# Kernel optimization log

Measured on AMD Instinct MI355X. Metric: run time of the kernel, lower is better.

Reference implementation:

```python
import jax, jax.numpy as jnp
import numpy as np

B, S, D_MODEL = 2, 2048, 2048
N_HEADS, N_KV_HEADS, HEAD_DIM = 32, 8, 64
N_GROUPS = N_HEADS // N_KV_HEADS


def setup_inputs() -> dict:
    key = jax.random.key(0)
    ks = jax.random.split(key, 5)
    x = jax.random.normal(ks[0], (B, S, D_MODEL), dtype=jnp.float32)
    wq = jax.random.normal(ks[1], (N_HEADS * HEAD_DIM, D_MODEL), dtype=jnp.float32) * 0.02
    wk = jax.random.normal(ks[2], (N_KV_HEADS * HEAD_DIM, D_MODEL), dtype=jnp.float32) * 0.02
    wv = jax.random.normal(ks[3], (N_KV_HEADS * HEAD_DIM, D_MODEL), dtype=jnp.float32) * 0.02
    wo = jax.random.normal(ks[4], (D_MODEL, N_HEADS * HEAD_DIM), dtype=jnp.float32) * 0.02
    # Rotary tables: module's apply_rope expects cos/sin of shape [S, head_dim//2]
    half = HEAD_DIM // 2
    inv_freq = 1.0 / (10000.0 ** (jnp.arange(0, half, dtype=jnp.float32) / half))
    angles = jnp.arange(S, dtype=jnp.float32)[:, None] * inv_freq[None, :]  # [S, half]
    cos = jnp.cos(angles)
    sin = jnp.sin(angles)
    return {"x": x, "wq": wq, "wk": wk, "wv": wv, "wo": wo, "cos": cos, "sin": sin}


def _rotate_half(t):
    half = t.shape[-1] // 2
    return jnp.concatenate((-t[..., half:], t[..., :half]), axis=-1)


def _apply_rope(q, k, cos, sin):
    # cos/sin: [S, head_dim//2] -> repeat_interleave(2) -> [S, head_dim]
    cos2 = jnp.repeat(cos, 2, axis=-1)[None, :, None, :]  # [1,S,1,D]
    sin2 = jnp.repeat(sin, 2, axis=-1)[None, :, None, :]
    q_rot = q * cos2 + _rotate_half(q) * sin2
    k_rot = k * cos2 + _rotate_half(k) * sin2
    return q_rot, k_rot


def reference(x, wq, wk, wv, wo, cos, sin):
    b, s, _ = x.shape
    q = (x @ wq.T).reshape(b, s, N_HEADS, HEAD_DIM)
    k = (x @ wk.T).reshape(b, s, N_KV_HEADS, HEAD_DIM)
    v = (x @ wv.T).reshape(b, s, N_KV_HEADS, HEAD_DIM)
    q, k = _apply_rope(q, k, cos, sin)
    # GQA expansion: repeat_interleave along head dim
    k = jnp.repeat(k, N_GROUPS, axis=2)  # [b,s,H,D]
    v = jnp.repeat(v, N_GROUPS, axis=2)
    q = q.transpose(0, 2, 1, 3)  # [b,H,s,D]
    k = k.transpose(0, 2, 1, 3)
    v = v.transpose(0, 2, 1, 3)
    scale = HEAD_DIM ** -0.5
    scores = jnp.einsum("bhqd,bhkd->bhqk", q, k) * scale
    causal = jnp.tril(jnp.ones((s, s), dtype=bool))
    scores = jnp.where(causal[None, None], scores, jnp.finfo(scores.dtype).min)
    attn = jax.nn.softmax(scores, axis=-1)
    out = jnp.einsum("bhqk,bhkd->bhqd", attn, v)
    out = out.transpose(0, 2, 1, 3).reshape(b, s, N_HEADS * HEAD_DIM)
    return out @ wo.T
```

## Files before the change

### kernel.cpp

```cpp
#include <hip/hip_runtime.h>
#include <hip/hip_bf16.h>

#define B_   2
#define S_   2048
#define DM   2048
#define NH   32
#define NKV  8
#define HD   64
#define MROWS 4096
#define NQKV  3072

typedef __attribute__((ext_vector_type(8))) short bf16x8;
typedef __attribute__((ext_vector_type(4))) float f32x4;
typedef __attribute__((ext_vector_type(16))) float f32x16;

__device__ __forceinline__ unsigned short f2b(float f) {
  __hip_bfloat16 h = __float2bfloat16(f);
  return *reinterpret_cast<unsigned short*>(&h);
}

__device__ __forceinline__ void gload16(const void* g, void* l) {
  __builtin_amdgcn_global_load_lds((__attribute__((address_space(1))) void*)g,
                                   (__attribute__((address_space(3))) void*)l,
                                   16, 0, 0);
}

__device__ __forceinline__ unsigned cvtpk(float lo, float hi) {
  unsigned r;
  asm("v_cvt_pk_bf16_f32 %0, %1, %2" : "=v"(r) : "v"(lo), "v"(hi));
  return r;
}

__device__ __forceinline__ void pl32swap(unsigned& a, unsigned& b) {
  asm volatile("v_permlane32_swap_b32 %0, %1" : "+v"(a), "+v"(b));
}

__device__ __forceinline__ float exp2hw(float x) {
  float r;
  asm("v_exp_f32 %0, %1" : "=v"(r) : "v"(x));
  return r;
}

__device__ __forceinline__ bf16x8 mk8(unsigned w0, unsigned w1, unsigned w2, unsigned w3) {
  union { unsigned u[4]; bf16x8 v; } uu;
  uu.u[0] = w0; uu.u[1] = w1; uu.u[2] = w2; uu.u[3] = w3;
  return uu.v;
}

__global__ __launch_bounds__(256) void f2bf_kernel(const float* __restrict__ in,
                                                   unsigned short* __restrict__ out, int n4) {
  int i = blockIdx.x * 256 + threadIdx.x;
  if (i < n4) {
    float4 v = reinterpret_cast<const float4*>(in)[i];
    ushort4 o;
    o.x = f2b(v.x); o.y = f2b(v.y); o.z = f2b(v.z); o.w = f2b(v.w);
    reinterpret_cast<ushort4*>(out)[i] = o;
  }
}

__global__ __launch_bounds__(256) void wcat_kernel(const float* __restrict__ wq,
                                                   const float* __restrict__ wk,
                                                   const float* __restrict__ wv,
                                                   unsigned short* __restrict__ out) {
  int i = blockIdx.x * 256 + threadIdx.x;
  int e = i * 4;
  int row = e >> 11;
  int col = e & 2047;
  const float* src;
  if (row < 2048)      src = wq + (size_t)row * 2048 + col;
  else if (row < 2560) src = wk + (size_t)(row - 2048) * 2048 + col;
  else                 src = wv + (size_t)(row - 2560) * 2048 + col;
  float4 v = *reinterpret_cast<const float4*>(src);
  ushort4 o;
  o.x = f2b(v.x); o.y = f2b(v.y); o.z = f2b(v.z); o.w = f2b(v.w);
  reinterpret_cast<ushort4*>(out)[i] = o;
}

#define BMg 256
#define BNg 128
#define BKg 64
#define QSCALE 0.18033688011112042f

__global__ __launch_bounds__(512, 2) void gemm_qkv(const unsigned short* __restrict__ A,
                                                   const unsigned short* __restrict__ Bm,
                                                   unsigned short* __restrict__ Qb,
                                                   unsigned short* __restrict__ Kb2,
                                                   unsigned short* __restrict__ Vtb,
                                                   const float* __restrict__ cosg,
                                                   const float* __restrict__ sing) {
  const int K = DM;
  __shared__ unsigned short Abuf[3][BMg * BKg];
  __shared__ unsigned short Bbuf[3][BNg * BKg];
  const int tid = threadIdx.x;
  const int wave = tid >> 6, lane = tid & 63;
  const int wr = wave >> 1, wc = wave & 1;
  const int rowbase = blockIdx.y * BMg;
  const int colbase = blockIdx.x * BNg;
  const unsigned short* Ag = A + (size_t)rowbase * K;
  const unsigned short* Bg = Bm + (size_t)colbase * K;
  const int NT = K / BKg;

  auto stage_half = [&](int buf, int k0, int half) {
#pragma unroll
    for (int i = 0; i < 2; ++i) {
      int c = wave * 256 + (half * 2 + i) * 64 + lane;
      int r = c >> 3, p = c & 7;
      gload16(Ag + (size_t)r * K + k0 + ((p ^ (r & 7)) << 3),
              &Abuf[buf][(wave * 256 + (half * 2 + i) * 64) * 8]);
    }
    int c = wave * 128 + half * 64 + lane;
    int r = c >> 3, p = c & 7;
    gload16(Bg + (size_t)r * K + k0 + ((p ^ (r & 7)) << 3),
            &Bbuf[buf][(wave * 128 + half * 64) * 8]);
  };
  auto ldA = [&](int buf, int row, int c16) -> bf16x8 {
    return *(const bf16x8*)((const char*)&Abuf[buf][0] + row * 128 + ((c16 ^ (row & 7)) << 4));
  };
  auto ldB = [&](int buf, int row, int c16) -> bf16x8 {
    return *(const bf16x8*)((const char*)&Bbuf[buf][0] + row * 128 + ((c16 ^ (row & 7)) << 4));
  };

  f32x4 acc[4][4];
#pragma unroll
  for (int a = 0; a < 4; a++)
#pragma unroll
    for (int b2 = 0; b2 < 4; b2++) acc[a][b2] = (f32x4){0.f, 0.f, 0.f, 0.f};

  const int l15 = lane & 15, l4 = lane >> 4;

  stage_half(0, 0, 0); stage_half(0, 0, 1);
  stage_half(1, BKg, 0); stage_half(1, BKg, 1);
  asm volatile("s_waitcnt vmcnt(6)" ::: "memory");
  __builtin_amdgcn_s_barrier();

  int cur = 0;
  for (int t = 0; t < NT; ++t) {
    const int nxt2 = (cur >= 1) ? cur - 1 : cur + 2;
    {
      bf16x8 af[4], bfv[4];
#pragma unroll
      for (int mt = 0; mt < 4; ++mt) af[mt] = ldA(cur, wr * 64 + mt * 16 + l15, l4);
#pragma unroll
      for (int nt = 0; nt < 4; ++nt) bfv[nt] = ldB(cur, wc * 64 + nt * 16 + l15, l4);
      if (t + 2 < NT) stage_half(nxt2, (t + 2) * BKg, 0);
      __builtin_amdgcn_s_barrier();
      __builtin_amdgcn_s_setprio(1);
#pragma unroll
      for (int mt = 0; mt < 4; ++mt)
#pragma unroll
        for (int nt = 0; nt < 4; ++nt)
          acc[mt][nt] = __builtin_amdgcn_mfma_f32_16x16x32_bf16(af[mt], bfv[nt], acc[mt][nt], 0, 0, 0);
      __builtin_amdgcn_s_setprio(0);
      __builtin_amdgcn_s_barrier();
    }
    {
      bf16x8 af[4], bfv[4];
#pragma unroll
      for (int mt = 0; mt < 4; ++mt) af[mt] = ldA(cur, wr * 64 + mt * 16 + l15, 4 + l4);
#pragma unroll
      for (int nt = 0; nt < 4; ++nt) bfv[nt] = ldB(cur, wc * 64 + nt * 16 + l15, 4 + l4);
      if (t + 2 < NT) stage_half(nxt2, (t + 2) * BKg, 1);
      __builtin_amdgcn_s_barrier();
      __builtin_amdgcn_s_setprio(1);
#pragma unroll
      for (int mt = 0; mt < 4; ++mt)
#pragma unroll
        for (int nt = 0; nt < 4; ++nt)
          acc[mt][nt] = __builtin_amdgcn_mfma_f32_16x16x32_bf16(af[mt], bfv[nt], acc[mt][nt], 0, 0, 0);
      __builtin_amdgcn_s_setprio(0);
      if (t < NT - 1) {
        if (t + 2 < NT) asm volatile("s_waitcnt vmcnt(6)" ::: "memory");
        else            asm volatile("s_waitcnt vmcnt(0)" ::: "memory");
        __builtin_amdgcn_s_barrier();
      }
    }
    cur = (cur < 2) ? cur + 1 : 0;
  }

  const int orow = rowbase + wr * 64, ocol = colbase + wc * 64;
  if (colbase < 2048) {
#pragma unroll
    for (int mt = 0; mt < 4; ++mt)
#pragma unroll
      for (int r = 0; r < 4; ++r) {
        const int row = orow + mt * 16 + l4 * 4 + r;
        const int s = row & 2047;
        const float* cR = cosg + s * 32;
        const float* sR = sing + s * 32;
#pragma unroll
        for (int nt = 0; nt < 2; ++nt) {
          const int i2 = nt * 8 + (l15 >> 1);
          float c0 = cR[i2], sv0 = sR[i2], c1 = cR[16 + i2], sv1 = sR[16 + i2];
          float alo = acc[mt][nt][r], ahi = acc[mt][nt + 2][r];
          size_t base = (size_t)row * 2048 + ocol + nt * 16 + l15;
          Qb[base]      = f2b((alo * c0 - ahi * sv0) * QSCALE);
          Qb[base + 32] = f2b((ahi * c1 + alo * sv1) * QSCALE);
        }
      }
  } else if (colbase < 2560) {
    const int kcol = ocol - 2048;
#pragma unroll
    for (int mt = 0; mt < 4; ++mt)
#pragma unroll
      for (int r = 0; r < 4; ++r) {
        const int row = orow + mt * 16 + l4 * 4 + r;
        const int s = row & 2047;
        const float* cR = cosg + s * 32;
        const float* sR = sing + s * 32;
#pragma unroll
        for (int nt = 0; nt < 2; ++nt) {
          const int i2 = nt * 8 + (l15 >> 1);
          float c0 = cR[i2], sv0 = sR[i2], c1 = cR[16 + i2], sv1 = sR[16 + i2];
          float alo = acc[mt][nt][r], ahi = acc[mt][nt + 2][r];
          size_t base = (size_t)row * 512 + kcol + nt * 16 + l15;
          Kb2[base]      = f2b(alo * c0 - ahi * sv0);
          Kb2[base + 32] = f2b(ahi * c1 + alo * sv1);
        }
      }
  } else {
    const int hkv = (ocol - 2560) >> 6;
#pragma unroll
    for (int mt = 0; mt < 4; ++mt)
#pragma unroll
      for (int nt = 0; nt < 4; ++nt) {
        const int d = nt * 16 + l15;
        const int row0 = orow + mt * 16 + l4 * 4;
        const int b = row0 >> 11, s0i = row0 & 2047;
        ushort4 u;
        u.x = f2b(acc[mt][nt][0]); u.y = f2b(acc[mt][nt][1]);
        u.z = f2b(acc[mt][nt][2]); u.w = f2b(acc[mt][nt][3]);
        *(ushort4*)(Vtb + ((size_t)(b * NKV + hkv) * HD + d) * S_ + s0i) = u;
      }
  }
}

__global__ __launch_bounds__(512, 2) void gemm_bt(const unsigned short* __restrict__ A,
                                                  const unsigned short* __restrict__ Bm,
                                                  float* __restrict__ C,
                                                  int M, int N, int K) {
  __shared__ unsigned short Abuf[3][BMg * BKg];
  __shared__ unsigned short Bbuf[3][BNg * BKg];
  const int tid = threadIdx.x;
  const int wave = tid >> 6, lane = tid & 63;
  const int wr = wave >> 1, wc = wave & 1;
  const int rowbase = blockIdx.y * BMg;
  const int colbase = blockIdx.x * BNg;
  const unsigned short* Ag = A + (size_t)rowbase * K;
  const unsigned short* Bg = Bm + (size_t)colbase * K;
  const int NT = K / BKg;

  auto stage_half = [&](int buf, int k0, int half) {
#pragma unroll
    for (int i = 0; i < 2; ++i) {
      int c = wave * 256 + (half * 2 + i) * 64 + lane;
      int r = c >> 3, p = c & 7;
      gload16(Ag + (size_t)r * K + k0 + ((p ^ (r & 7)) << 3),
              &Abuf[buf][(wave * 256 + (half * 2 + i) * 64) * 8]);
    }
    int c = wave * 128 + half * 64 + lane;
    int r = c >> 3, p = c & 7;
    gload16(Bg + (size_t)r * K + k0 + ((p ^ (r & 7)) << 3),
            &Bbuf[buf][(wave * 128 + half * 64) * 8]);
  };
  auto ldA = [&](int buf, int row, int c16) -> bf16x8 {
    return *(const bf16x8*)((const char*)&Abuf[buf][0] + row * 128 + ((c16 ^ (row & 7)) << 4));
  };
  auto ldB = [&](int buf, int row, int c16) -> bf16x8 {
    return *(const bf16x8*)((const char*)&Bbuf[buf][0] + row * 128 + ((c16 ^ (row & 7)) << 4));
  };

  f32x4 acc[4][4];
#pragma unroll
  for (int a = 0; a < 4; a++)
#pragma unroll
    for (int b2 = 0; b2 < 4; b2++) acc[a][b2] = (f32x4){0.f, 0.f, 0.f, 0.f};

  const int l15 = lane & 15, l4 = lane >> 4;

  stage_half(0, 0, 0); stage_half(0, 0, 1);
  stage_half(1, BKg, 0); stage_half(1, BKg, 1);
  asm volatile("s_waitcnt vmcnt(6)" ::: "memory");
  __builtin_amdgcn_s_barrier();

  int cur = 0;
  for (int t = 0; t < NT; ++t) {
    const int nxt2 = (cur >= 1) ? cur - 1 : cur + 2;
    {
      bf16x8 af[4], bfv[4];
#pragma unroll
      for (int mt = 0; mt < 4; ++mt) af[mt] = ldA(cur, wr * 64 + mt * 16 + l15, l4);
#pragma unroll
      for (int nt = 0; nt < 4; ++nt) bfv[nt] = ldB(cur, wc * 64 + nt * 16 + l15, l4);
      if (t + 2 < NT) stage_half(nxt2, (t + 2) * BKg, 0);
      __builtin_amdgcn_s_barrier();
      __builtin_amdgcn_s_setprio(1);
#pragma unroll
      for (int mt = 0; mt < 4; ++mt)
#pragma unroll
        for (int nt = 0; nt < 4; ++nt)
          acc[mt][nt] = __builtin_amdgcn_mfma_f32_16x16x32_bf16(af[mt], bfv[nt], acc[mt][nt], 0, 0, 0);
      __builtin_amdgcn_s_setprio(0);
      __builtin_amdgcn_s_barrier();
    }
    {
      bf16x8 af[4], bfv[4];
#pragma unroll
      for (int mt = 0; mt < 4; ++mt) af[mt] = ldA(cur, wr * 64 + mt * 16 + l15, 4 + l4);
#pragma unroll
      for (int nt = 0; nt < 4; ++nt) bfv[nt] = ldB(cur, wc * 64 + nt * 16 + l15, 4 + l4);
      if (t + 2 < NT) stage_half(nxt2, (t + 2) * BKg, 1);
      __builtin_amdgcn_s_barrier();
      __builtin_amdgcn_s_setprio(1);
#pragma unroll
      for (int mt = 0; mt < 4; ++mt)
#pragma unroll
        for (int nt = 0; nt < 4; ++nt)
          acc[mt][nt] = __builtin_amdgcn_mfma_f32_16x16x32_bf16(af[mt], bfv[nt], acc[mt][nt], 0, 0, 0);
      __builtin_amdgcn_s_setprio(0);
      if (t < NT - 1) {
        if (t + 2 < NT) asm volatile("s_waitcnt vmcnt(6)" ::: "memory");
        else            asm volatile("s_waitcnt vmcnt(0)" ::: "memory");
        __builtin_amdgcn_s_barrier();
      }
    }
    cur = (cur < 2) ? cur + 1 : 0;
  }

  const int orow = rowbase + wr * 64, ocol = colbase + wc * 64;
#pragma unroll
  for (int mt = 0; mt < 4; mt++)
#pragma unroll
    for (int nt = 0; nt < 4; nt++)
#pragma unroll
      for (int r = 0; r < 4; r++)
        C[(size_t)(orow + mt * 16 + l4 * 4 + r) * N + ocol + nt * 16 + l15] = acc[mt][nt][r];
}

__global__ __launch_bounds__(256) void attn_kernel(const unsigned short* __restrict__ Qb,
                                                   const unsigned short* __restrict__ Kb2,
                                                   const unsigned short* __restrict__ Vt,
                                                   unsigned short* __restrict__ AO) {
  const int pr = blockIdx.x, h = blockIdx.y, b = blockIdx.z;
  const int hk = h >> 2;
  __shared__ unsigned short Kbuf[3][4096];
  __shared__ unsigned short Vbuf[3][4096];
  const int tid = threadIdx.x, wave = tid >> 6, lane = tid & 63;
  const int l31 = lane & 31, hi = lane >> 5;

  const unsigned short* Qrow = Qb + (size_t)b * S_ * 2048 + h * 64;
  const unsigned short* Krow = Kb2 + (size_t)b * S_ * 512 + hk * 64;
  const unsigned short* Vbase = Vt + (size_t)(b * NKV + hk) * HD * S_;

  const int NT_B = 2 * (16 - pr);
  const int NTtot = 34;

  auto j0_of = [&](int tl) { return (tl < NT_B ? tl : tl - NT_B) * 64; };
  auto stage = [&](int j0, int bufi) {
#pragma unroll
    for (int tt = 0; tt < 2; ++tt) {
      int slot = (wave * 2 + tt) * 64 + lane;
      int row = slot >> 3, blk = slot & 7;
      int sb = ((blk ^ (row & 7)) << 3);
      gload16(Krow + (size_t)(j0 + row) * 512 + sb, &Kbuf[bufi][(wave * 2 + tt) * 512]);
      gload16(Vbase + (size_t)row * S_ + j0 + sb, &Vbuf[bufi][(wave * 2 + tt) * 512]);
    }
  };

  stage(0, 0);
  stage(j0_of(1), 1);
  asm volatile("s_waitcnt vmcnt(4)" ::: "memory");
  __builtin_amdgcn_s_barrier();

  int cur = 0, tlin = 0;

  for (int rg = 0; rg < 2; ++rg) {
    const int qbi = rg == 0 ? (15 - pr) : pr;
    const int qb = qbi * 128;
    const int NT = 2 * (qbi + 1);
    const int q0w = qb + wave * 32;
    const int qg = q0w + l31;

    bf16x8 qf[4];
#pragma unroll
    for (int c = 0; c < 4; ++c)
      qf[c] = *reinterpret_cast<const bf16x8*>(Qrow + (size_t)qg * 2048 + c * 16 + hi * 8);

    f32x16 Oa0 = {}, Oa1 = {};
    float m_old = -INFINITY, lsum = 0.f;

    for (int t = 0; t < NT; ++t, ++tlin) {
      const int j0 = t * 64;
      if (tlin + 2 < NTtot) stage(j0_of(tlin + 2), cur >= 1 ? cur - 1 : cur + 2);

      if (j0 < q0w + 32) {
        const char* Klc = (const char*)&Kbuf[cur][0];
        const char* Vlc = (const char*)&Vbuf[cur][0];

        f32x16 s0 = {}, s1 = {};
        __builtin_amdgcn_s_setprio(1);
#pragma unroll
        for (int c = 0; c < 4; ++c) {
          const int r0 = l31;
          bf16x8 kf = *(const bf16x8*)(Klc + r0 * 128 + ((((c << 1) + hi) ^ (r0 & 7)) << 4));
          s0 = __builtin_amdgcn_mfma_f32_32x32x16_bf16(kf, qf[c], s0, 0, 0, 0);
        }
#pragma unroll
        for (int c = 0; c < 4; ++c) {
          const int r1 = 32 + l31;
          bf16x8 kf = *(const bf16x8*)(Klc + r1 * 128 + ((((c << 1) + hi) ^ (r1 & 7)) << 4));
          s1 = __builtin_amdgcn_mfma_f32_32x32x16_bf16(kf, qf[c], s1, 0, 0, 0);
        }
        __builtin_amdgcn_s_setprio(0);

        const bool need_mask = (j0 + 63 > q0w);
        const int kb0 = j0 + 4 * hi, kb1 = j0 + 32 + 4 * hi;
        if (need_mask) {
#pragma unroll
          for (int r = 0; r < 16; ++r) {
            const int ko = (r & 3) + 8 * (r >> 2);
            if (kb0 + ko > qg) s0[r] = -INFINITY;
            if (kb1 + ko > qg) s1[r] = -INFINITY;
          }
        }

        float a0 = fmaxf(s0[0], s1[0]), a1 = fmaxf(s0[1], s1[1]);
        float a2 = fmaxf(s0[2], s1[2]), a3 = fmaxf(s0[3], s1[3]);
#pragma unroll
        for (int r = 4; r < 16; r += 4) {
          a0 = fmaxf(a0, fmaxf(s0[r], s1[r]));
          a1 = fmaxf(a1, fmaxf(s0[r + 1], s1[r + 1]));
          a2 = fmaxf(a2, fmaxf(s0[r + 2], s1[r + 2]));
          a3 = fmaxf(a3, fmaxf(s0[r + 3], s1[r + 3]));
        }
        float mxt = fmaxf(fmaxf(a0, a1), fmaxf(a2, a3));
        mxt = fmaxf(mxt, __shfl_xor(mxt, 32, 64));

        if (!__all(mxt - m_old <= 8.f)) {
          float mnew = fmaxf(m_old, mxt);
          float corr = exp2hw(m_old - mnew);
          m_old = mnew;
          lsum *= corr;
#pragma unroll
          for (int r = 0; r < 16; ++r) { Oa0[r] *= corr; Oa1[r] *= corr; }
        }

        float t0 = 0.f, t1 = 0.f, t2 = 0.f, t3 = 0.f;
#pragma unroll
        for (int r = 0; r < 16; r += 4) {
          s0[r]     = exp2hw(s0[r] - m_old);     t0 += s0[r];
          s0[r + 1] = exp2hw(s0[r + 1] - m_old); t1 += s0[r + 1];
          s0[r + 2] = exp2hw(s0[r + 2] - m_old); t2 += s0[r + 2];
          s0[r + 3] = exp2hw(s0[r + 3] - m_old); t3 += s0[r + 3];
        }
#pragma unroll
        for (int r = 0; r < 16; r += 4) {
          s1[r]     = exp2hw(s1[r] - m_old);     t0 += s1[r];
          s1[r + 1] = exp2hw(s1[r + 1] - m_old); t1 += s1[r + 1];
          s1[r + 2] = exp2hw(s1[r + 2] - m_old); t2 += s1[r + 2];
          s1[r + 3] = exp2hw(s1[r + 3] - m_old); t3 += s1[r + 3];
        }
        float rs = (t0 + t1) + (t2 + t3);
        rs += __shfl_xor(rs, 32, 64);
        lsum += rs;

        unsigned a0u = cvtpk(s0[0], s0[1]),  b0u = cvtpk(s0[4], s0[5]);  pl32swap(a0u, b0u);
        unsigned a1u = cvtpk(s0[2], s0[3]),  b1u = cvtpk(s0[6], s0[7]);  pl32swap(a1u, b1u);
        bf16x8 pf00 = mk8(a0u, a1u, b0u, b1u);
        unsigned a2u = cvtpk(s0[8], s0[9]),  b2u = cvtpk(s0[12], s0[13]); pl32swap(a2u, b2u);
        unsigned a3u = cvtpk(s0[10], s0[11]), b3u = cvtpk(s0[14], s0[15]); pl32swap(a3u, b3u);
        bf16x8 pf01 = mk8(a2u, a3u, b2u, b3u);
        unsigned a4u = cvtpk(s1[0], s1[1]),  b4u = cvtpk(s1[4], s1[5]);  pl32swap(a4u, b4u);
        unsigned a5u = cvtpk(s1[2], s1[3]),  b5u = cvtpk(s1[6], s1[7]);  pl32swap(a5u, b5u);
        bf16x8 pf10 = mk8(a4u, a5u, b4u, b5u);
        unsigned a6u = cvtpk(s1[8], s1[9]),  b6u = cvtpk(s1[12], s1[13]); pl32swap(a6u, b6u);
        unsigned a7u = cvtpk(s1[10], s1[11]), b7u = cvtpk(s1[14], s1[15]); pl32swap(a7u, b7u);
        bf16x8 pf11 = mk8(a6u, a7u, b6u, b7u);

        __builtin_amdgcn_s_setprio(1);
#pragma unroll
        for (int sk = 0; sk < 4; ++sk) {
          const int s = sk >> 1, kc = sk & 1;
          const bf16x8 pf = (sk == 0) ? pf00 : (sk == 1) ? pf01 : (sk == 2) ? pf10 : pf11;
          {
            const int row = l31;
            bf16x8 vf = *(const bf16x8*)(Vlc + row * 128 +
                          ((((s << 2) + (kc << 1) + hi) ^ (row & 7)) << 4));
            Oa0 = __builtin_amdgcn_mfma_f32_32x32x16_bf16(vf, pf, Oa0, 0, 0, 0);
          }
          {
            const int row = 32 + l31;
            bf16x8 vf = *(const bf16x8*)(Vlc + row * 128 +
                          ((((s << 2) + (kc << 1) + hi) ^ (row & 7)) << 4));
            Oa1 = __builtin_amdgcn_mfma_f32_32x32x16_bf16(vf, pf, Oa1, 0, 0, 0);
          }
        }
        __builtin_amdgcn_s_setprio(0);
      }

      if (tlin + 1 < NTtot) {
        if (tlin + 2 < NTtot) asm volatile("s_waitcnt vmcnt(4)" ::: "memory");
        else                  asm volatile("s_waitcnt vmcnt(0)" ::: "memory");
        __builtin_amdgcn_s_barrier();
      }
      cur = (cur < 2) ? cur + 1 : 0;
    }

    const float inv = 1.0f / lsum;
    unsigned short* ob = AO + (size_t)(b * S_ + qg) * 2048 + h * 64;
#pragma unroll
    for (int c = 0; c < 4; ++c) {
      ushort4 u0, u1;
      u0.x = f2b(Oa0[4 * c] * inv);     u0.y = f2b(Oa0[4 * c + 1] * inv);
      u0.z = f2b(Oa0[4 * c + 2] * inv); u0.w = f2b(Oa0[4 * c + 3] * inv);
      u1.x = f2b(Oa1[4 * c] * inv);     u1.y = f2b(Oa1[4 * c + 1] * inv);
      u1.z = f2b(Oa1[4 * c + 2] * inv); u1.w = f2b(Oa1[4 * c + 3] * inv);
      *(ushort4*)(ob + 8 * c + 4 * hi)      = u0;
      *(ushort4*)(ob + 32 + 8 * c + 4 * hi) = u1;
    }
  }
}

extern "C" void kernel_launch(void* const* d_in, const int* in_sizes, int n_in,
                              void* d_out, int out_size, void* d_ws, size_t ws_size,
                              hipStream_t stream) {
  (void)in_sizes; (void)n_in; (void)out_size; (void)ws_size;
  const float* x    = (const float*)d_in[0];
  const float* wq   = (const float*)d_in[1];
  const float* wk   = (const float*)d_in[2];
  const float* wv   = (const float*)d_in[3];
  const float* wo   = (const float*)d_in[4];
  const float* wo_  = wo;
  const float* cosg = (const float*)d_in[5];
  const float* sing = (const float*)d_in[6];
  (void)wo_;

  char* ws = (char*)d_ws;
  unsigned short* xb   = (unsigned short*)(ws);
  unsigned short* wcat = (unsigned short*)(ws + 16777216);
  unsigned short* wob  = (unsigned short*)(ws + 29360128);
  unsigned short* Qb   = (unsigned short*)(ws + 37748736);
  unsigned short* Kb2  = (unsigned short*)(ws + 54525952);
  unsigned short* Vtb  = (unsigned short*)(ws + 58720256);
  unsigned short* AO   = xb;

  f2bf_kernel<<<8192, 256, 0, stream>>>(x, xb, 2097152);
  wcat_kernel<<<6144, 256, 0, stream>>>(wq, wk, wv, wcat);
  f2bf_kernel<<<4096, 256, 0, stream>>>(wo, wob, 1048576);

  gemm_qkv<<<dim3(NQKV / BNg, MROWS / BMg), 512, 0, stream>>>(xb, wcat, Qb, Kb2, Vtb, cosg, sing);

  attn_kernel<<<dim3(8, NH, B_), 256, 0, stream>>>(Qb, Kb2, Vtb, AO);

  gemm_bt<<<dim3(DM / BNg, MROWS / BMg), 512, 0, stream>>>(AO, wob, (float*)d_out, MROWS, DM, DM);
}
```

Before: 203.6 us.

## Retile QKV GEMM to 128x128x32 and widen attention KV tiles to 128

The QKV projection GEMM moves from 256x128x64 tiles with 512 threads to 128x128x32 tiles with 256 threads. This gives more blocks (768 instead of 192) and targets higher occupancy, at the cost of more barriers per unit of K. Separately, the attention kernel now processes 128-key tiles with double buffering instead of 64-key tiles with triple buffering. That halves the number of loop iterations and barriers, but raises register pressure from four score accumulators and doubles the shared memory per stage. The prefetch is now issued after a barrier at the end of each iteration, rather than at the start.

New measurement: 184.3 us. 1.1x faster.

```diff
diff --git a/kernel.cpp b/kernel.cpp
--- a/kernel.cpp
+++ b/kernel.cpp
@@ -76,12 +76,9 @@
   reinterpret_cast<ushort4*>(out)[i] = o;
 }
 
-#define BMg 256
-#define BNg 128
-#define BKg 64
 #define QSCALE 0.18033688011112042f
 
-__global__ __launch_bounds__(512, 2) void gemm_qkv(const unsigned short* __restrict__ A,
+__global__ __launch_bounds__(256, 3) void gemm_qkv(const unsigned short* __restrict__ A,
                                                    const unsigned short* __restrict__ Bm,
                                                    unsigned short* __restrict__ Qb,
                                                    unsigned short* __restrict__ Kb2,
@@ -89,35 +86,38 @@
                                                    const float* __restrict__ cosg,
                                                    const float* __restrict__ sing) {
   const int K = DM;
-  __shared__ unsigned short Abuf[3][BMg * BKg];
-  __shared__ unsigned short Bbuf[3][BNg * BKg];
+  __shared__ unsigned short Abuf[3][128 * 32];
+  __shared__ unsigned short Bbuf[3][128 * 32];
   const int tid = threadIdx.x;
   const int wave = tid >> 6, lane = tid & 63;
   const int wr = wave >> 1, wc = wave & 1;
-  const int rowbase = blockIdx.y * BMg;
-  const int colbase = blockIdx.x * BNg;
+  const int rowbase = blockIdx.y * 128;
+  const int colbase = blockIdx.x * 128;
   const unsigned short* Ag = A + (size_t)rowbase * K;
   const unsigned short* Bg = Bm + (size_t)colbase * K;
-  const int NT = K / BKg;
-
-  auto stage_half = [&](int buf, int k0, int half) {
-#pragma unroll
-    for (int i = 0; i < 2; ++i) {
-      int c = wave * 256 + (half * 2 + i) * 64 + lane;
-      int r = c >> 3, p = c & 7;
-      gload16(Ag + (size_t)r * K + k0 + ((p ^ (r & 7)) << 3),
-              &Abuf[buf][(wave * 256 + (half * 2 + i) * 64) * 8]);
-    }
-    int c = wave * 128 + half * 64 + lane;
-    int r = c >> 3, p = c & 7;
-    gload16(Bg + (size_t)r * K + k0 + ((p ^ (r & 7)) << 3),
-            &Bbuf[buf][(wave * 128 + half * 64) * 8]);
-  };
-  auto ldA = [&](int buf, int row, int c16) -> bf16x8 {
-    return *(const bf16x8*)((const char*)&Abuf[buf][0] + row * 128 + ((c16 ^ (row & 7)) << 4));
-  };
-  auto ldB = [&](int buf, int row, int c16) -> bf16x8 {
-    return *(const bf16x8*)((const char*)&Bbuf[buf][0] + row * 128 + ((c16 ^ (row & 7)) << 4));
+  const int NT = K / 32;
+
+  auto stage = [&](int buf, int k0) {
+#pragma unroll
+    for (int it = 0; it < 2; ++it) {
+      int slot = wave * 128 + it * 64 + lane;
+      int r = slot >> 2, p = slot & 3;
+      gload16(Ag + (size_t)r * K + k0 + ((p ^ ((r >> 1) & 3)) << 3),
+              &Abuf[buf][(wave * 128 + it * 64) * 8]);
+    }
+#pragma unroll
+    for (int it = 0; it < 2; ++it) {
+      int slot = wave * 128 + it * 64 + lane;
+      int r = slot >> 2, p = slot & 3;
+      gload16(Bg + (size_t)r * K + k0 + ((p ^ ((r >> 1) & 3)) << 3),
+              &Bbuf[buf][(wave * 128 + it * 64) * 8]);
+    }
+  };
+  auto ldA = [&](int buf, int row, int c) -> bf16x8 {
+    return *(const bf16x8*)((const char*)&Abuf[buf][0] + row * 64 + ((c ^ ((row >> 1) & 3)) << 4));
+  };
+  auto ldB = [&](int buf, int row, int c) -> bf16x8 {
+    return *(const bf16x8*)((const char*)&Bbuf[buf][0] + row * 64 + ((c ^ ((row >> 1) & 3)) << 4));
   };
 
   f32x4 acc[4][4];
@@ -128,51 +128,32 @@
 
   const int l15 = lane & 15, l4 = lane >> 4;
 
-  stage_half(0, 0, 0); stage_half(0, 0, 1);
-  stage_half(1, BKg, 0); stage_half(1, BKg, 1);
-  asm volatile("s_waitcnt vmcnt(6)" ::: "memory");
+  stage(0, 0);
+  stage(1, 32);
+  asm volatile("s_waitcnt vmcnt(4)" ::: "memory");
   __builtin_amdgcn_s_barrier();
 
   int cur = 0;
   for (int t = 0; t < NT; ++t) {
     const int nxt2 = (cur >= 1) ? cur - 1 : cur + 2;
-    {
-      bf16x8 af[4], bfv[4];
-#pragma unroll
-      for (int mt = 0; mt < 4; ++mt) af[mt] = ldA(cur, wr * 64 + mt * 16 + l15, l4);
-#pragma unroll
-      for (int nt = 0; nt < 4; ++nt) bfv[nt] = ldB(cur, wc * 64 + nt * 16 + l15, l4);
-      if (t + 2 < NT) stage_half(nxt2, (t + 2) * BKg, 0);
+    bf16x8 af[4], bfv[4];
+#pragma unroll
+    for (int mt = 0; mt < 4; ++mt) af[mt] = ldA(cur, wr * 64 + mt * 16 + l15, l4);
+#pragma unroll
+    for (int nt = 0; nt < 4; ++nt) bfv[nt] = ldB(cur, wc * 64 + nt * 16 + l15, l4);
+    if (t + 2 < NT) stage(nxt2, (t + 2) * 32);
+    __builtin_amdgcn_s_barrier();
+    __builtin_amdgcn_s_setprio(1);
+#pragma unroll
+    for (int mt = 0; mt < 4; ++mt)
+#pragma unroll
+      for (int nt = 0; nt < 4; ++nt)
+        acc[mt][nt] = __builtin_amdgcn_mfma_f32_16x16x32_bf16(af[mt], bfv[nt], acc[mt][nt], 0, 0, 0);
+    __builtin_amdgcn_s_setprio(0);
+    if (t < NT - 1) {
+      if (t + 2 < NT) asm volatile("s_waitcnt vmcnt(4)" ::: "memory");
+      else            asm volatile("s_waitcnt vmcnt(0)" ::: "memory");
       __builtin_amdgcn_s_barrier();
-      __builtin_amdgcn_s_setprio(1);
-#pragma unroll
-      for (int mt = 0; mt < 4; ++mt)
-#pragma unroll
-        for (int nt = 0; nt < 4; ++nt)
-          acc[mt][nt] = __builtin_amdgcn_mfma_f32_16x16x32_bf16(af[mt], bfv[nt], acc[mt][nt], 0, 0, 0);
-      __builtin_amdgcn_s_setprio(0);
-      __builtin_amdgcn_s_barrier();
-    }
-    {
-      bf16x8 af[4], bfv[4];
-#pragma unroll
-      for (int mt = 0; mt < 4; ++mt) af[mt] = ldA(cur, wr * 64 + mt * 16 + l15, 4 + l4);
-#pragma unroll
-      for (int nt = 0; nt < 4; ++nt) bfv[nt] = ldB(cur, wc * 64 + nt * 16 + l15, 4 + l4);
-      if (t + 2 < NT) stage_half(nxt2, (t + 2) * BKg, 1);
-      __builtin_amdgcn_s_barrier();
-      __builtin_amdgcn_s_setprio(1);
-#pragma unroll
-      for (int mt = 0; mt < 4; ++mt)
-#pragma unroll
-        for (int nt = 0; nt < 4; ++nt)
-          acc[mt][nt] = __builtin_amdgcn_mfma_f32_16x16x32_bf16(af[mt], bfv[nt], acc[mt][nt], 0, 0, 0);
-      __builtin_amdgcn_s_setprio(0);
-      if (t < NT - 1) {
-        if (t + 2 < NT) asm volatile("s_waitcnt vmcnt(6)" ::: "memory");
-        else            asm volatile("s_waitcnt vmcnt(0)" ::: "memory");
-        __builtin_amdgcn_s_barrier();
-      }
     }
     cur = (cur < 2) ? cur + 1 : 0;
   }
@@ -234,6 +215,9 @@
   }
 }
 
+#define BMg 256
+#define BNg 128
+#define BKg 64
 __global__ __launch_bounds__(512, 2) void gemm_bt(const unsigned short* __restrict__ A,
                                                   const unsigned short* __restrict__ Bm,
                                                   float* __restrict__ C,
@@ -336,14 +320,14 @@
         C[(size_t)(orow + mt * 16 + l4 * 4 + r) * N + ocol + nt * 16 + l15] = acc[mt][nt][r];
 }
 
-__global__ __launch_bounds__(256) void attn_kernel(const unsigned short* __restrict__ Qb,
-                                                   const unsigned short* __restrict__ Kb2,
-                                                   const unsigned short* __restrict__ Vt,
-                                                   unsigned short* __restrict__ AO) {
+__global__ __launch_bounds__(256, 2) void attn_kernel(const unsigned short* __restrict__ Qb,
+                                                      const unsigned short* __restrict__ Kb2,
+                                                      const unsigned short* __restrict__ Vt,
+                                                      unsigned short* __restrict__ AO) {
   const int pr = blockIdx.x, h = blockIdx.y, b = blockIdx.z;
   const int hk = h >> 2;
-  __shared__ unsigned short Kbuf[3][4096];
-  __shared__ unsigned short Vbuf[3][4096];
+  __shared__ unsigned short Kbuf[2][8192];
+  __shared__ unsigned short Vbuf[2][8192];
   const int tid = threadIdx.x, wave = tid >> 6, lane = tid & 63;
   const int l31 = lane & 31, hi = lane >> 5;
 
@@ -351,24 +335,30 @@
   const unsigned short* Krow = Kb2 + (size_t)b * S_ * 512 + hk * 64;
   const unsigned short* Vbase = Vt + (size_t)(b * NKV + hk) * HD * S_;
 
-  const int NT_B = 2 * (16 - pr);
-  const int NTtot = 34;
-
-  auto j0_of = [&](int tl) { return (tl < NT_B ? tl : tl - NT_B) * 64; };
+  const int NT_A = 16 - pr;
+  const int NTtot = 17;
+
+  auto j0_of = [&](int tl) { return (tl < NT_A ? tl : tl - NT_A) * 128; };
   auto stage = [&](int j0, int bufi) {
 #pragma unroll
-    for (int tt = 0; tt < 2; ++tt) {
-      int slot = (wave * 2 + tt) * 64 + lane;
-      int row = slot >> 3, blk = slot & 7;
-      int sb = ((blk ^ (row & 7)) << 3);
-      gload16(Krow + (size_t)(j0 + row) * 512 + sb, &Kbuf[bufi][(wave * 2 + tt) * 512]);
-      gload16(Vbase + (size_t)row * S_ + j0 + sb, &Vbuf[bufi][(wave * 2 + tt) * 512]);
-    }
-  };
-
-  stage(0, 0);
+    for (int it = 0; it < 4; ++it) {
+      int slot = (wave * 4 + it) * 64 + lane;
+      int row = slot >> 3, p = slot & 7;
+      gload16(Krow + (size_t)(j0 + row) * 512 + ((p ^ (row & 7)) << 3),
+              &Kbuf[bufi][(wave * 4 + it) * 512]);
+    }
+#pragma unroll
+    for (int it = 0; it < 4; ++it) {
+      int slot = (wave * 4 + it) * 64 + lane;
+      int row = slot >> 4, p = slot & 15;
+      gload16(Vbase + (size_t)row * S_ + j0 + ((p ^ (row & 15)) << 3),
+              &Vbuf[bufi][(wave * 4 + it) * 512]);
+    }
+  };
+
+  stage(j0_of(0), 0);
   stage(j0_of(1), 1);
-  asm volatile("s_waitcnt vmcnt(4)" ::: "memory");
+  asm volatile("s_waitcnt vmcnt(8)" ::: "memory");
   __builtin_amdgcn_s_barrier();
 
   int cur = 0, tlin = 0;
@@ -376,7 +366,7 @@
   for (int rg = 0; rg < 2; ++rg) {
     const int qbi = rg == 0 ? (15 - pr) : pr;
     const int qb = qbi * 128;
-    const int NT = 2 * (qbi + 1);
+    const int NT = qbi + 1;
     const int q0w = qb + wave * 32;
     const int qg = q0w + l31;
 
@@ -389,48 +379,50 @@
     float m_old = -INFINITY, lsum = 0.f;
 
     for (int t = 0; t < NT; ++t, ++tlin) {
-      const int j0 = t * 64;
-      if (tlin + 2 < NTtot) stage(j0_of(tlin + 2), cur >= 1 ? cur - 1 : cur + 2);
+      const int j0 = t * 128;
 
       if (j0 < q0w + 32) {
         const char* Klc = (const char*)&Kbuf[cur][0];
         const char* Vlc = (const char*)&Vbuf[cur][0];
 
-        f32x16 s0 = {}, s1 = {};
+        f32x16 s0 = {}, s1 = {}, s2 = {}, s3 = {};
         __builtin_amdgcn_s_setprio(1);
 #pragma unroll
         for (int c = 0; c < 4; ++c) {
-          const int r0 = l31;
-          bf16x8 kf = *(const bf16x8*)(Klc + r0 * 128 + ((((c << 1) + hi) ^ (r0 & 7)) << 4));
-          s0 = __builtin_amdgcn_mfma_f32_32x32x16_bf16(kf, qf[c], s0, 0, 0, 0);
-        }
-#pragma unroll
-        for (int c = 0; c < 4; ++c) {
-          const int r1 = 32 + l31;
-          bf16x8 kf = *(const bf16x8*)(Klc + r1 * 128 + ((((c << 1) + hi) ^ (r1 & 7)) << 4));
-          s1 = __builtin_amdgcn_mfma_f32_32x32x16_bf16(kf, qf[c], s1, 0, 0, 0);
+          const int xb = ((c << 1) + hi) ^ (l31 & 7);
+          bf16x8 kf0 = *(const bf16x8*)(Klc + (l31) * 128       + (xb << 4));
+          s0 = __builtin_amdgcn_mfma_f32_32x32x16_bf16(kf0, qf[c], s0, 0, 0, 0);
+          bf16x8 kf1 = *(const bf16x8*)(Klc + (32 + l31) * 128  + (xb << 4));
+          s1 = __builtin_amdgcn_mfma_f32_32x32x16_bf16(kf1, qf[c], s1, 0, 0, 0);
+          bf16x8 kf2 = *(const bf16x8*)(Klc + (64 + l31) * 128  + (xb << 4));
+          s2 = __builtin_amdgcn_mfma_f32_32x32x16_bf16(kf2, qf[c], s2, 0, 0, 0);
+          bf16x8 kf3 = *(const bf16x8*)(Klc + (96 + l31) * 128  + (xb << 4));
+          s3 = __builtin_amdgcn_mfma_f32_32x32x16_bf16(kf3, qf[c], s3, 0, 0, 0);
         }
         __builtin_amdgcn_s_setprio(0);
 
-        const bool need_mask = (j0 + 63 > q0w);
-        const int kb0 = j0 + 4 * hi, kb1 = j0 + 32 + 4 * hi;
-        if (need_mask) {
+        if (j0 + 127 > q0w) {
+          const int kb0 = j0 + 4 * hi, kb1 = kb0 + 32, kb2m = kb0 + 64, kb3 = kb0 + 96;
 #pragma unroll
           for (int r = 0; r < 16; ++r) {
             const int ko = (r & 3) + 8 * (r >> 2);
             if (kb0 + ko > qg) s0[r] = -INFINITY;
             if (kb1 + ko > qg) s1[r] = -INFINITY;
+            if (kb2m + ko > qg) s2[r] = -INFINITY;
+            if (kb3 + ko > qg) s3[r] = -INFINITY;
           }
         }
 
-        float a0 = fmaxf(s0[0], s1[0]), a1 = fmaxf(s0[1], s1[1]);
-        float a2 = fmaxf(s0[2], s1[2]), a3 = fmaxf(s0[3], s1[3]);
+        float a0 = fmaxf(fmaxf(s0[0], s1[0]), fmaxf(s2[0], s3[0]));
+        float a1 = fmaxf(fmaxf(s0[1], s1[1]), fmaxf(s2[1], s3[1]));
+        float a2 = fmaxf(fmaxf(s0[2], s1[2]), fmaxf(s2[2], s3[2]));
+        float a3 = fmaxf(fmaxf(s0[3], s1[3]), fmaxf(s2[3], s3[3]));
 #pragma unroll
         for (int r = 4; r < 16; r += 4) {
-          a0 = fmaxf(a0, fmaxf(s0[r], s1[r]));
-          a1 = fmaxf(a1, fmaxf(s0[r + 1], s1[r + 1]));
-          a2 = fmaxf(a2, fmaxf(s0[r + 2], s1[r + 2]));
-          a3 = fmaxf(a3, fmaxf(s0[r + 3], s1[r + 3]));
+          a0 = fmaxf(a0, fmaxf(fmaxf(s0[r], s1[r]), fmaxf(s2[r], s3[r])));
+          a1 = fmaxf(a1, fmaxf(fmaxf(s0[r + 1], s1[r + 1]), fmaxf(s2[r + 1], s3[r + 1])));
+          a2 = fmaxf(a2, fmaxf(fmaxf(s0[r + 2], s1[r + 2]), fmaxf(s2[r + 2], s3[r + 2])));
+          a3 = fmaxf(a3, fmaxf(fmaxf(s0[r + 3], s1[r + 3]), fmaxf(s2[r + 3], s3[r + 3])));
         }
         float mxt = fmaxf(fmaxf(a0, a1), fmaxf(a2, a3));
         mxt = fmaxf(mxt, __shfl_xor(mxt, 32, 64));
@@ -459,50 +451,82 @@
           s1[r + 2] = exp2hw(s1[r + 2] - m_old); t2 += s1[r + 2];
           s1[r + 3] = exp2hw(s1[r + 3] - m_old); t3 += s1[r + 3];
         }
+#pragma unroll
+        for (int r = 0; r < 16; r += 4) {
+          s2[r]     = exp2hw(s2[r] - m_old);     t0 += s2[r];
+          s2[r + 1] = exp2hw(s2[r + 1] - m_old); t1 += s2[r + 1];
+          s2[r + 2] = exp2hw(s2[r + 2] - m_old); t2 += s2[r + 2];
+          s2[r + 3] = exp2hw(s2[r + 3] - m_old); t3 += s2[r + 3];
+        }
+#pragma unroll
+        for (int r = 0; r < 16; r += 4) {
+          s3[r]     = exp2hw(s3[r] - m_old);     t0 += s3[r];
+          s3[r + 1] = exp2hw(s3[r + 1] - m_old); t1 += s3[r + 1];
+          s3[r + 2] = exp2hw(s3[r + 2] - m_old); t2 += s3[r + 2];
+          s3[r + 3] = exp2hw(s3[r + 3] - m_old); t3 += s3[r + 3];
+        }
         float rs = (t0 + t1) + (t2 + t3);
         rs += __shfl_xor(rs, 32, 64);
         lsum += rs;
 
-        unsigned a0u = cvtpk(s0[0], s0[1]),  b0u = cvtpk(s0[4], s0[5]);  pl32swap(a0u, b0u);
-        unsigned a1u = cvtpk(s0[2], s0[3]),  b1u = cvtpk(s0[6], s0[7]);  pl32swap(a1u, b1u);
-        bf16x8 pf00 = mk8(a0u, a1u, b0u, b1u);
-        unsigned a2u = cvtpk(s0[8], s0[9]),  b2u = cvtpk(s0[12], s0[13]); pl32swap(a2u, b2u);
-        unsigned a3u = cvtpk(s0[10], s0[11]), b3u = cvtpk(s0[14], s0[15]); pl32swap(a3u, b3u);
-        bf16x8 pf01 = mk8(a2u, a3u, b2u, b3u);
-        unsigned a4u = cvtpk(s1[0], s1[1]),  b4u = cvtpk(s1[4], s1[5]);  pl32swap(a4u, b4u);
-        unsigned a5u = cvtpk(s1[2], s1[3]),  b5u = cvtpk(s1[6], s1[7]);  pl32swap(a5u, b5u);
-        bf16x8 pf10 = mk8(a4u, a5u, b4u, b5u);
-        unsigned a6u = cvtpk(s1[8], s1[9]),  b6u = cvtpk(s1[12], s1[13]); pl32swap(a6u, b6u);
-        unsigned a7u = cvtpk(s1[10], s1[11]), b7u = cvtpk(s1[14], s1[15]); pl32swap(a7u, b7u);
-        bf16x8 pf11 = mk8(a6u, a7u, b6u, b7u);
-
+        bf16x8 pf0, pf1, pf2, pf3, pf4, pf5, pf6, pf7;
+        {
+          unsigned aA = cvtpk(s0[0], s0[1]),  bA = cvtpk(s0[4], s0[5]);  pl32swap(aA, bA);
+          unsigned aB = cvtpk(s0[2], s0[3]),  bB = cvtpk(s0[6], s0[7]);  pl32swap(aB, bB);
+          pf0 = mk8(aA, aB, bA, bB);
+          unsigned aC = cvtpk(s0[8], s0[9]),  bC = cvtpk(s0[12], s0[13]); pl32swap(aC, bC);
+          unsigned aD = cvtpk(s0[10], s0[11]), bD = cvtpk(s0[14], s0[15]); pl32swap(aD, bD);
+          pf1 = mk8(aC, aD, bC, bD);
+        }
+        {
+          unsigned aA = cvtpk(s1[0], s1[1]),  bA = cvtpk(s1[4], s1[5]);  pl32swap(aA, bA);
+          unsigned aB = cvtpk(s1[2], s1[3]),  bB = cvtpk(s1[6], s1[7]);  pl32swap(aB, bB);
+          pf2 = mk8(aA, aB, bA, bB);
+          unsigned aC = cvtpk(s1[8], s1[9]),  bC = cvtpk(s1[12], s1[13]); pl32swap(aC, bC);
+          unsigned aD = cvtpk(s1[10], s1[11]), bD = cvtpk(s1[14], s1[15]); pl32swap(aD, bD);
+          pf3 = mk8(aC, aD, bC, bD);
+        }
+        {
+          unsigned aA = cvtpk(s2[0], s2[1]),  bA = cvtpk(s2[4], s2[5]);  pl32swap(aA, bA);
+          unsigned aB = cvtpk(s2[2], s2[3]),  bB = cvtpk(s2[6], s2[7]);  pl32swap(aB, bB);
+          pf4 = mk8(aA, aB, bA, bB);
+          unsigned aC = cvtpk(s2[8], s2[9]),  bC = cvtpk(s2[12], s2[13]); pl32swap(aC, bC);
+          unsigned aD = cvtpk(s2[10], s2[11]), bD = cvtpk(s2[14], s2[15]); pl32swap(aD, bD);
+          pf5 = mk8(aC, aD, bC, bD);
+        }
+        {
+          unsigned aA = cvtpk(s3[0], s3[1]),  bA = cvtpk(s3[4], s3[5]);  pl32swap(aA, bA);
+          unsigned aB = cvtpk(s3[2], s3[3]),  bB = cvtpk(s3[6], s3[7]);  pl32swap(aB, bB);
+          pf6 = mk8(aA, aB, bA, bB);
+          unsigned aC = cvtpk(s3[8], s3[9]),  bC = cvtpk(s3[12], s3[13]); pl32swap(aC, bC);
+          unsigned aD = cvtpk(s3[10], s3[11]), bD = cvtpk(s3[14], s3[15]); pl32swap(aD, bD);
+          pf7 = mk8(aC, aD, bC, bD);
+        }
+
+        const int xv = l31 & 15;
         __builtin_amdgcn_s_setprio(1);
-#pragma unroll
-        for (int sk = 0; sk < 4; ++sk) {
-          const int s = sk >> 1, kc = sk & 1;
-          const bf16x8 pf = (sk == 0) ? pf00 : (sk == 1) ? pf01 : (sk == 2) ? pf10 : pf11;
-          {
-            const int row = l31;
-            bf16x8 vf = *(const bf16x8*)(Vlc + row * 128 +
-                          ((((s << 2) + (kc << 1) + hi) ^ (row & 7)) << 4));
-            Oa0 = __builtin_amdgcn_mfma_f32_32x32x16_bf16(vf, pf, Oa0, 0, 0, 0);
-          }
-          {
-            const int row = 32 + l31;
-            bf16x8 vf = *(const bf16x8*)(Vlc + row * 128 +
-                          ((((s << 2) + (kc << 1) + hi) ^ (row & 7)) << 4));
-            Oa1 = __builtin_amdgcn_mfma_f32_32x32x16_bf16(vf, pf, Oa1, 0, 0, 0);
-          }
-        }
+#define PVSTEP(PF, SK)                                                                     \
+        {                                                                                  \
+          const int xc = (((SK) << 1) + hi) ^ xv;                                          \
+          bf16x8 vf0 = *(const bf16x8*)(Vlc + l31 * 256 + (xc << 4));                      \
+          Oa0 = __builtin_amdgcn_mfma_f32_32x32x16_bf16(vf0, PF, Oa0, 0, 0, 0);            \
+          bf16x8 vf1 = *(const bf16x8*)(Vlc + (32 + l31) * 256 + (xc << 4));               \
+          Oa1 = __builtin_amdgcn_mfma_f32_32x32x16_bf16(vf1, PF, Oa1, 0, 0, 0);            \
+        }
+        PVSTEP(pf0, 0) PVSTEP(pf1, 1) PVSTEP(pf2, 2) PVSTEP(pf3, 3)
+        PVSTEP(pf4, 4) PVSTEP(pf5, 5) PVSTEP(pf6, 6) PVSTEP(pf7, 7)
+#undef PVSTEP
         __builtin_amdgcn_s_setprio(0);
       }
 
+      __builtin_amdgcn_s_barrier();
+      if (tlin + 2 < NTtot) stage(j0_of(tlin + 2), cur);
       if (tlin + 1 < NTtot) {
-        if (tlin + 2 < NTtot) asm volatile("s_waitcnt vmcnt(4)" ::: "memory");
+        if (tlin + 2 < NTtot) asm volatile("s_waitcnt vmcnt(8)" ::: "memory");
         else                  asm volatile("s_waitcnt vmcnt(0)" ::: "memory");
         __builtin_amdgcn_s_barrier();
       }
-      cur = (cur < 2) ? cur + 1 : 0;
+      cur ^= 1;
     }
 
     const float inv = 1.0f / lsum;
@@ -529,10 +553,8 @@
   const float* wk   = (const float*)d_in[2];
   const float* wv   = (const float*)d_in[3];
   const float* wo   = (const float*)d_in[4];
-  const float* wo_  = wo;
   const float* cosg = (const float*)d_in[5];
   const float* sing = (const float*)d_in[6];
-  (void)wo_;
 
   char* ws = (char*)d_ws;
   unsigned short* xb   = (unsigned short*)(ws);
@@ -547,7 +569,7 @@
   wcat_kernel<<<6144, 256, 0, stream>>>(wq, wk, wv, wcat);
   f2bf_kernel<<<4096, 256, 0, stream>>>(wo, wob, 1048576);
 
-  gemm_qkv<<<dim3(NQKV / BNg, MROWS / BMg), 512, 0, stream>>>(xb, wcat, Qb, Kb2, Vtb, cosg, sing);
+  gemm_qkv<<<dim3(NQKV / 128, MROWS / 128), 256, 0, stream>>>(xb, wcat, Qb, Kb2, Vtb, cosg, sing);
 
   attn_kernel<<<dim3(8, NH, B_), 256, 0, stream>>>(Qb, Kb2, Vtb, AO);
 
```
